# Kernel tuning notes

Measured on AMD Instinct MI355X. Metric: run time of the kernel, lower is better.

## Reference

```python
import jax, jax.numpy as jnp
import numpy as np

KITTI_MAX_DISTANCE = 80.0  # scale factor applied to normalized range values


def _pairwise_sqdist(a, b):
    # a: [B, N, 3], b: [B, M, 3] -> [B, N, M] squared euclidean distances
    a2 = jnp.sum(a * a, axis=-1)  # [B, N]
    b2 = jnp.sum(b * b, axis=-1)  # [B, M]
    ab = jnp.einsum('bnd,bmd->bnm', a, b)  # [B, N, M]
    d2 = a2[:, :, None] + b2[:, None, :] - 2.0 * ab
    return jnp.maximum(d2, 0.0)


def chamfer_distance(p1, p2):
    # kaolin-style: per-batch mean of squared NN distances, both directions
    d2 = _pairwise_sqdist(p1, p2)           # [B, N, M]
    d_p1 = jnp.min(d2, axis=2)              # [B, N] pred -> gt
    d_p2 = jnp.min(d2, axis=1)              # [B, M] gt -> pred
    return jnp.mean(d_p1, axis=1) + jnp.mean(d_p2, axis=1)  # [B]


def setup_inputs() -> dict:
    key = jax.random.key(0)
    k1, k2 = jax.random.split(key)
    B, N, M = 2, 8192, 8192
    image_pred = jax.random.normal(k1, (B, N, 3), dtype=jnp.float32)
    image_gt = jax.random.normal(k2, (B, M, 3), dtype=jnp.float32)
    return {"image_pred": image_pred, "image_gt": image_gt}


def reference(image_pred, image_gt):
    # scale normalized coordinates to metric space (as in the original forward)
    pred = image_pred * KITTI_MAX_DISTANCE
    gt = image_gt * KITTI_MAX_DISTANCE
    cd = chamfer_distance(pred[:, :, :3], gt[:, :, :3])  # [B]
    # 0.7 * filtered + 0.3 * non-filtered collapses to a single mean when no
    # data-dependent label filtering is applied (weights sum to 1.0)
    return jnp.mean(cd)
```

## Files before the change

kernel.cpp:

```cpp
#include <hip/hip_runtime.h>
#include <hip/hip_bf16.h>
#include <stdint.h>


typedef __attribute__((ext_vector_type(8))) short short8v;
typedef __attribute__((ext_vector_type(16))) float f32x16;

#define NP 8192
#define NCHUNK 4
#define CHUNKCOLS 2048
#define NT 64
#define SCALE 0.390625f

#define OFF_ROW 0u
#define OFF_A   1048576u
#define OFF_B   2097152u

__device__ inline uint32_t f2u(float f){ union{float f;uint32_t u;}c; c.f=f; return c.u; }
__device__ inline float u2f(uint32_t u){ union{float f;uint32_t u;}c; c.u=u; return c.f; }
__device__ inline uint16_t bfr(float f){ uint32_t u=f2u(f); return (uint16_t)((u + 0x7FFFu + ((u>>16)&1u))>>16); }
__device__ inline float bff(uint16_t s){ return u2f(((uint32_t)s)<<16); }
__device__ inline float min3f(float a,float b,float c){ return fminf(fminf(a,b),c); }

__device__ inline void packA(float x, float y, float z, ushort* dst) {
  const uint16_t hx=bfr(x), hy=bfr(y), hz=bfr(z);
  const uint16_t lx=bfr(x-bff(hx)), ly=bfr(y-bff(hy)), lz=bfr(z-bff(hz));
  const float s2 = fmaf(x,x,fmaf(y,y,z*z));
  const uint16_t h2=bfr(s2), l2=bfr(s2-bff(h2));
  union{ ushort u[16]; uint4 v[2]; } A;
  A.u[0]=bfr(-2.f*bff(hx)); A.u[1]=bfr(-2.f*bff(hy)); A.u[2]=bfr(-2.f*bff(hz));
  A.u[3]=A.u[0]; A.u[4]=A.u[1]; A.u[5]=A.u[2];
  A.u[6]=bfr(-2.f*bff(lx)); A.u[7]=bfr(-2.f*bff(ly)); A.u[8]=bfr(-2.f*bff(lz));
  A.u[9]=A.u[6]; A.u[10]=A.u[7]; A.u[11]=A.u[8];
  A.u[12]=h2; A.u[13]=l2; A.u[14]=0x3F80; A.u[15]=0x3F80;
  ((uint4*)dst)[0]=A.v[0]; ((uint4*)dst)[1]=A.v[1];
}

__device__ inline void packB(float x, float y, float z, ushort* dst) {
  const uint16_t hx=bfr(x), hy=bfr(y), hz=bfr(z);
  const uint16_t lx=bfr(x-bff(hx)), ly=bfr(y-bff(hy)), lz=bfr(z-bff(hz));
  const float s2 = fmaf(x,x,fmaf(y,y,z*z));
  const uint16_t h2=bfr(s2), l2=bfr(s2-bff(h2));
  union{ ushort u[16]; uint4 v[2]; } B;
  B.u[0]=hx; B.u[1]=hy; B.u[2]=hz; B.u[3]=lx; B.u[4]=ly; B.u[5]=lz;
  B.u[6]=hx; B.u[7]=hy; B.u[8]=hz; B.u[9]=lx; B.u[10]=ly; B.u[11]=lz;
  B.u[12]=0x3F80; B.u[13]=0x3F80; B.u[14]=h2; B.u[15]=l2;
  ((uint4*)dst)[0]=B.v[0]; ((uint4*)dst)[1]=B.v[1];
}

__global__ __launch_bounds__(256) void prep_kernel(
    const float* __restrict__ pred, const float* __restrict__ gt,
    float* __restrict__ out, uint8_t* __restrict__ ws) {
  const int tid = blockIdx.x*256 + (int)threadIdx.x;
  if (tid == 0) out[0] = 0.0f;
  const int b = tid >> 13, i = tid & 8191;
  const float* p = pred + ((size_t)b*NP + i)*3;
  const float* g = gt   + ((size_t)b*NP + i)*3;
  const float px=p[0], py=p[1], pz=p[2];
  const float gx=g[0], gy=g[1], gz=g[2];
  ushort* A = (ushort*)(ws + OFF_A);
  ushort* Bp = (ushort*)(ws + OFF_B);
  packA(px,py,pz, A  + ((size_t)(0*2+b)*NP + i)*16);
  packB(gx,gy,gz, Bp + ((size_t)(0*2+b)*NP + i)*16);
  packA(gx,gy,gz, A  + ((size_t)(1*2+b)*NP + i)*16);
  packB(px,py,pz, Bp + ((size_t)(1*2+b)*NP + i)*16);
}

__global__ __launch_bounds__(256) void chamfer_mfma_kernel(uint8_t* __restrict__ ws) {
  const int wave = threadIdx.x >> 6, lane = threadIdx.x & 63;
  const int half = lane >> 5, l31 = lane & 31;
  const int stripe = blockIdx.x*4 + wave;
  const int chunk  = blockIdx.y;
  const int db     = blockIdx.z;

  const ushort* PA = (const ushort*)(ws + OFF_A) + (size_t)db*NP*16;
  const ushort* PB = (const ushort*)(ws + OFF_B) + (size_t)db*NP*16;
  float* WROW = (float*)(ws + OFF_ROW);

  const int arow = stripe*32 + l31;
  const short8v afrag = *(const short8v*)(PA + (size_t)arow*16 + half*8);

  const ushort* pb0 = PB + ((size_t)(chunk*CHUNKCOLS + l31))*16 + half*8;
#define LDB(ct) (*(const short8v*)(pb0 + (size_t)(ct)*512))

  const f32x16 zero = {};
  float rowmin[16];
#pragma unroll
  for (int i=0;i<16;++i) rowmin[i] = 3.4e38f;

  short8v bA=LDB(0), bB=LDB(1), bC=LDB(2), bD=LDB(3);
#pragma unroll 2
  for (int tp=0; tp<NT/2; ++tp) {
    const int t0 = 2*tp;
    const short8v nA = LDB((t0+4)&(NT-1));
    const short8v nB = LDB((t0+5)&(NT-1));
    const f32x16 aA = __builtin_amdgcn_mfma_f32_32x32x16_bf16(afrag, bA, zero, 0,0,0);
    const f32x16 aB = __builtin_amdgcn_mfma_f32_32x32x16_bf16(afrag, bB, zero, 0,0,0);
#pragma unroll
    for (int i=0;i<16;++i) rowmin[i] = min3f(rowmin[i], aA[i], aB[i]);
    bA=bC; bB=bD; bC=nA; bD=nB;
  }
#undef LDB

#pragma unroll
  for (int i=0;i<16;++i) {
    float v = rowmin[i];
    v = fminf(v, __shfl_xor(v, 1));
    v = fminf(v, __shfl_xor(v, 2));
    v = fminf(v, __shfl_xor(v, 4));
    v = fminf(v, __shfl_xor(v, 8));
    v = fminf(v, __shfl_xor(v, 16));
    rowmin[i] = v;
  }
  if (l31 == 0) {
    float* wr = WROW + ((size_t)db*NCHUNK + chunk)*NP + stripe*32 + half*4;
#pragma unroll
    for (int i=0;i<16;++i) wr[(i&3) + 8*(i>>2)] = rowmin[i];
  }
}

__global__ __launch_bounds__(256) void reduce_kernel(
    const uint8_t* __restrict__ ws, float* __restrict__ out) {
  const float* WROW = (const float*)(ws + OFF_ROW);
  const int tid = blockIdx.x*256 + (int)threadIdx.x;
  const int db = tid >> 13, q = tid & 8191;

  const float* pr = WROW + (size_t)db*NCHUNK*NP + q;
  const float m0 = fminf(pr[0], pr[NP]);
  const float m1 = fminf(pr[2*NP], pr[3*NP]);
  float sum = fmaxf(fminf(m0, m1), 0.0f);

#pragma unroll
  for (int off=32; off>0; off>>=1) sum += __shfl_down(sum, off);
  __shared__ float red[4];
  if ((threadIdx.x & 63) == 0) red[threadIdx.x >> 6] = sum;
  __syncthreads();
  if (threadIdx.x == 0) atomicAdd(out, (red[0]+red[1]+red[2]+red[3]) * SCALE);
}

extern "C" void kernel_launch(void* const* d_in, const int* in_sizes, int n_in,
                              void* d_out, int out_size, void* d_ws, size_t ws_size,
                              hipStream_t stream) {
  const float* pred = (const float*)d_in[0];
  const float* gt = (const float*)d_in[1];
  float* out = (float*)d_out;
  uint8_t* ws = (uint8_t*)d_ws;

  prep_kernel<<<64, 256, 0, stream>>>(pred, gt, out, ws);
  chamfer_mfma_kernel<<<dim3(64, NCHUNK, 4), 256, 0, stream>>>(ws);
  reduce_kernel<<<128, 256, 0, stream>>>(ws, out);
}
```

Measured before the change: 30.48 us.

## Stage B tiles in LDS with double buffering and build A fragments in-kernel

The main kernel now computes the A-side bf16 split fragments directly from the raw point arrays, so prep no longer writes a packed A buffer. The B-side data is stored split into separate half planes and loaded cooperatively into a double-buffered shared-memory tile, so the four waves of a block share one global load per step instead of each wave streaming B from global memory. This cuts redundant global/L2 traffic but adds a __syncthreads per 128-column step, plus LDS read latency inside the MFMA loop.

```diff
diff --git a/kernel.cpp b/kernel.cpp
--- a/kernel.cpp
+++ b/kernel.cpp
@@ -9,12 +9,12 @@
 #define NP 8192
 #define NCHUNK 4
 #define CHUNKCOLS 2048
-#define NT 64
+#define NSTEP 128
+#define NSTEPS (CHUNKCOLS / NSTEP)
 #define SCALE 0.390625f
 
 #define OFF_ROW 0u
-#define OFF_A   1048576u
-#define OFF_B   2097152u
+#define OFF_B   1048576u
 
 __device__ inline uint32_t f2u(float f){ union{float f;uint32_t u;}c; c.f=f; return c.u; }
 __device__ inline float u2f(uint32_t u){ union{float f;uint32_t u;}c; c.u=u; return c.f; }
@@ -22,21 +22,19 @@
 __device__ inline float bff(uint16_t s){ return u2f(((uint32_t)s)<<16); }
 __device__ inline float min3f(float a,float b,float c){ return fminf(fminf(a,b),c); }
 
-__device__ inline void packA(float x, float y, float z, ushort* dst) {
-  const uint16_t hx=bfr(x), hy=bfr(y), hz=bfr(z);
-  const uint16_t lx=bfr(x-bff(hx)), ly=bfr(y-bff(hy)), lz=bfr(z-bff(hz));
-  const float s2 = fmaf(x,x,fmaf(y,y,z*z));
-  const uint16_t h2=bfr(s2), l2=bfr(s2-bff(h2));
-  union{ ushort u[16]; uint4 v[2]; } A;
-  A.u[0]=bfr(-2.f*bff(hx)); A.u[1]=bfr(-2.f*bff(hy)); A.u[2]=bfr(-2.f*bff(hz));
-  A.u[3]=A.u[0]; A.u[4]=A.u[1]; A.u[5]=A.u[2];
-  A.u[6]=bfr(-2.f*bff(lx)); A.u[7]=bfr(-2.f*bff(ly)); A.u[8]=bfr(-2.f*bff(lz));
-  A.u[9]=A.u[6]; A.u[10]=A.u[7]; A.u[11]=A.u[8];
-  A.u[12]=h2; A.u[13]=l2; A.u[14]=0x3F80; A.u[15]=0x3F80;
-  ((uint4*)dst)[0]=A.v[0]; ((uint4*)dst)[1]=A.v[1];
-}
+__global__ __launch_bounds__(256) void prep_kernel(
+    const float* __restrict__ pred, const float* __restrict__ gt,
+    float* __restrict__ out, uint8_t* __restrict__ ws) {
+  const int tid = blockIdx.x*256 + (int)threadIdx.x;
+  if (tid == 0) out[0] = 0.0f;
+  const int col  = tid & 8191;
+  const int half = (tid >> 13) & 1;
+  const int db   = tid >> 14;
+  const int dir = db >> 1, b = db & 1;
 
-__device__ inline void packB(float x, float y, float z, ushort* dst) {
+  const float* src = (dir == 0 ? gt : pred) + ((size_t)b*NP + col)*3;
+  const float x = src[0], y = src[1], z = src[2];
+
   const uint16_t hx=bfr(x), hy=bfr(y), hz=bfr(z);
   const uint16_t lx=bfr(x-bff(hx)), ly=bfr(y-bff(hy)), lz=bfr(z-bff(hz));
   const float s2 = fmaf(x,x,fmaf(y,y,z*z));
@@ -45,62 +43,72 @@
   B.u[0]=hx; B.u[1]=hy; B.u[2]=hz; B.u[3]=lx; B.u[4]=ly; B.u[5]=lz;
   B.u[6]=hx; B.u[7]=hy; B.u[8]=hz; B.u[9]=lx; B.u[10]=ly; B.u[11]=lz;
   B.u[12]=0x3F80; B.u[13]=0x3F80; B.u[14]=h2; B.u[15]=l2;
-  ((uint4*)dst)[0]=B.v[0]; ((uint4*)dst)[1]=B.v[1];
+
+  uint4* BP = (uint4*)(ws + OFF_B);
+  BP[(size_t)tid] = half ? B.v[1] : B.v[0];
 }
 
-__global__ __launch_bounds__(256) void prep_kernel(
+__global__ __launch_bounds__(256) void chamfer_mfma_kernel(
     const float* __restrict__ pred, const float* __restrict__ gt,
-    float* __restrict__ out, uint8_t* __restrict__ ws) {
-  const int tid = blockIdx.x*256 + (int)threadIdx.x;
-  if (tid == 0) out[0] = 0.0f;
-  const int b = tid >> 13, i = tid & 8191;
-  const float* p = pred + ((size_t)b*NP + i)*3;
-  const float* g = gt   + ((size_t)b*NP + i)*3;
-  const float px=p[0], py=p[1], pz=p[2];
-  const float gx=g[0], gy=g[1], gz=g[2];
-  ushort* A = (ushort*)(ws + OFF_A);
-  ushort* Bp = (ushort*)(ws + OFF_B);
-  packA(px,py,pz, A  + ((size_t)(0*2+b)*NP + i)*16);
-  packB(gx,gy,gz, Bp + ((size_t)(0*2+b)*NP + i)*16);
-  packA(gx,gy,gz, A  + ((size_t)(1*2+b)*NP + i)*16);
-  packB(px,py,pz, Bp + ((size_t)(1*2+b)*NP + i)*16);
-}
-
-__global__ __launch_bounds__(256) void chamfer_mfma_kernel(uint8_t* __restrict__ ws) {
+    uint8_t* __restrict__ ws) {
   const int wave = threadIdx.x >> 6, lane = threadIdx.x & 63;
   const int half = lane >> 5, l31 = lane & 31;
   const int stripe = blockIdx.x*4 + wave;
   const int chunk  = blockIdx.y;
   const int db     = blockIdx.z;
-
-  const ushort* PA = (const ushort*)(ws + OFF_A) + (size_t)db*NP*16;
-  const ushort* PB = (const ushort*)(ws + OFF_B) + (size_t)db*NP*16;
-  float* WROW = (float*)(ws + OFF_ROW);
+  const int dir = db >> 1, b = db & 1;
 
   const int arow = stripe*32 + l31;
-  const short8v afrag = *(const short8v*)(PA + (size_t)arow*16 + half*8);
+  const float* ap = (dir == 0 ? pred : gt) + ((size_t)b*NP + arow)*3;
+  short8v afrag;
+  {
+    const float x = ap[0], y = ap[1], z = ap[2];
+    const uint16_t hx=bfr(x), hy=bfr(y), hz=bfr(z);
+    const uint16_t lx=bfr(x-bff(hx)), ly=bfr(y-bff(hy)), lz=bfr(z-bff(hz));
+    const float s2 = fmaf(x,x,fmaf(y,y,z*z));
+    const uint16_t h2=bfr(s2), l2=bfr(s2-bff(h2));
+    const uint16_t nhx=bfr(-2.f*bff(hx)), nhy=bfr(-2.f*bff(hy)), nhz=bfr(-2.f*bff(hz));
+    const uint16_t nlx=bfr(-2.f*bff(lx)), nly=bfr(-2.f*bff(ly)), nlz=bfr(-2.f*bff(lz));
+    union{ ushort u[16]; short8v s8[2]; } A;
+    A.u[0]=nhx; A.u[1]=nhy; A.u[2]=nhz; A.u[3]=nhx; A.u[4]=nhy; A.u[5]=nhz;
+    A.u[6]=nlx; A.u[7]=nly; A.u[8]=nlz; A.u[9]=nlx; A.u[10]=nly; A.u[11]=nlz;
+    A.u[12]=h2; A.u[13]=l2; A.u[14]=0x3F80; A.u[15]=0x3F80;
+    afrag = half ? A.s8[1] : A.s8[0];
+  }
 
-  const ushort* pb0 = PB + ((size_t)(chunk*CHUNKCOLS + l31))*16 + half*8;
-#define LDB(ct) (*(const short8v*)(pb0 + (size_t)(ct)*512))
+  __shared__ uint4 lds[2][2][NSTEP];
+  const uint4* BP = (const uint4*)(ws + OFF_B) + (size_t)db*2*NP
+                    + (size_t)chunk*CHUNKCOLS;
+  const int st_half = threadIdx.x >> 7;
+  const int st_col  = threadIdx.x & 127;
 
-  const f32x16 zero = {};
   float rowmin[16];
 #pragma unroll
   for (int i=0;i<16;++i) rowmin[i] = 3.4e38f;
+  const f32x16 zero = {};
 
-  short8v bA=LDB(0), bB=LDB(1), bC=LDB(2), bD=LDB(3);
-#pragma unroll 2
-  for (int tp=0; tp<NT/2; ++tp) {
-    const int t0 = 2*tp;
-    const short8v nA = LDB((t0+4)&(NT-1));
-    const short8v nB = LDB((t0+5)&(NT-1));
-    const f32x16 aA = __builtin_amdgcn_mfma_f32_32x32x16_bf16(afrag, bA, zero, 0,0,0);
-    const f32x16 aB = __builtin_amdgcn_mfma_f32_32x32x16_bf16(afrag, bB, zero, 0,0,0);
+  lds[0][st_half][st_col] = BP[(size_t)st_half*NP + st_col];
+  __syncthreads();
+
+  int buf = 0;
+  for (int s = 0; s < NSTEPS; ++s) {
+    if (s + 1 < NSTEPS) {
+      lds[buf^1][st_half][st_col] =
+          BP[(size_t)st_half*NP + (s+1)*NSTEP + st_col];
+    }
+    const uint4* lrow = &lds[buf][half][0];
 #pragma unroll
-    for (int i=0;i<16;++i) rowmin[i] = min3f(rowmin[i], aA[i], aB[i]);
-    bA=bC; bB=bD; bC=nA; bD=nB;
+    for (int pr = 0; pr < 2; ++pr) {
+      const short8v b0 = *(const short8v*)&lrow[pr*64 + l31];
+      const short8v b1 = *(const short8v*)&lrow[pr*64 + 32 + l31];
+      const f32x16 a0 = __builtin_amdgcn_mfma_f32_32x32x16_bf16(afrag, b0, zero, 0,0,0);
+      const f32x16 a1 = __builtin_amdgcn_mfma_f32_32x32x16_bf16(afrag, b1, zero, 0,0,0);
+#pragma unroll
+      for (int i=0;i<16;++i) rowmin[i] = min3f(rowmin[i], a0[i], a1[i]);
+    }
+    __syncthreads();
+    buf ^= 1;
   }
-#undef LDB
 
 #pragma unroll
   for (int i=0;i<16;++i) {
@@ -113,7 +121,8 @@
     rowmin[i] = v;
   }
   if (l31 == 0) {
-    float* wr = WROW + ((size_t)db*NCHUNK + chunk)*NP + stripe*32 + half*4;
+    float* wr = (float*)(ws + OFF_ROW) + ((size_t)db*NCHUNK + chunk)*NP
+                + stripe*32 + half*4;
 #pragma unroll
     for (int i=0;i<16;++i) wr[(i&3) + 8*(i>>2)] = rowmin[i];
   }
@@ -146,7 +155,7 @@
   float* out = (float*)d_out;
   uint8_t* ws = (uint8_t*)d_ws;
 
-  prep_kernel<<<64, 256, 0, stream>>>(pred, gt, out, ws);
-  chamfer_mfma_kernel<<<dim3(64, NCHUNK, 4), 256, 0, stream>>>(ws);
+  prep_kernel<<<256, 256, 0, stream>>>(pred, gt, out, ws);
+  chamfer_mfma_kernel<<<dim3(NP/128, NCHUNK, 4), 256, 0, stream>>>(pred, gt, ws);
   reduce_kernel<<<128, 256, 0, stream>>>(ws, out);
 }
```

Result: slower. 41.44 us (+36.0%).
